# Optimization experiments

Hardware: AMD Instinct MI355X
Metric: run time of the kernel (lower is better)

Reference implementation:

```python
import jax, jax.numpy as jnp
import numpy as np

RADII = np.array([0.5, 1.0, 1.5, 2.0], dtype=np.float32)
SIGMA = 0.5          # gaussian radial-function width (= radius spacing)
EPS = 1e-8
N_SH = 9             # real spherical harmonics up to l=2
N_BASIS = len(RADII) * N_SH


def real_sh_l2(u):
    """Real spherical harmonics l=0,1,2 of unit vectors u[..., 3] -> [..., 9]."""
    x, y, z = u[..., 0], u[..., 1], u[..., 2]
    one = jnp.ones_like(x)
    return jnp.stack([
        0.28209479 * one,
        0.48860251 * x, 0.48860251 * y, 0.48860251 * z,
        1.09254843 * x * y,
        1.09254843 * y * z,
        0.31539157 * (3.0 * z * z - 1.0),
        1.09254843 * x * z,
        0.54627421 * (x * x - y * y),
    ], axis=-1)


def setup_inputs() -> dict:
    key = jax.random.key(0)
    k1, k2, k3, k4, k5 = jax.random.split(key, 5)
    n, c_in, d_out, b, a = 4, 32, 32, 8192, 32
    inp = jax.random.normal(k1, (n, c_in, b), jnp.float32)
    coords = jax.random.uniform(k2, (n, b, 3), jnp.float32) * 4.0
    neighbors = jax.random.randint(k3, (n, b, a), 0, b)
    relative_mask = jax.random.uniform(k4, (n, b, a), jnp.float32)
    W = jax.random.normal(k5, (d_out, c_in, N_BASIS), jnp.float32) / np.sqrt(c_in * N_BASIS)
    return {"input": inp, "coords": coords, "relative_mask": relative_mask,
            "W": W, "neighbors": neighbors}


def reference(input, coords, relative_mask, W, neighbors):
    n, c, b = input.shape
    idx_n = jnp.arange(n)[:, None, None]                     # [n,1,1]
    # neighbor difference matrix: coords[neighbors] - coords  -> [n,b,a,3]
    neigh_xyz = coords[idx_n, neighbors]
    diff = neigh_xyz - coords[:, :, None, :]
    r = jnp.linalg.norm(diff, axis=-1)                       # [n,b,a]
    u = diff / (r[..., None] + EPS)
    Y = real_sh_l2(u)                                        # [n,b,a,9]
    radii = jnp.asarray(RADII)
    rb = jnp.exp(-((r[..., None] - radii) / SIGMA) ** 2)     # [n,b,a,4]
    basis = (rb[..., :, None] * Y[..., None, :]).reshape(r.shape + (-1,))  # [n,b,a,36]
    # neighbor feature matrix: input[n, :, neighbors[n,b,a]] -> [n,b,a,c]
    feat = input[idx_n, :, neighbors]
    # relative_mask multiplies k over (n,b,a) == masking gathered features
    feat = feat * relative_mask[..., None]
    # fused form of: k[d,c,n,b,a] = sum_k basis[n,b,a,k] W[d,c,k];
    # out[n,d,b] = sum_{c,a} feat[n,b,a,c] * k[d,c,n,b,a]
    M = jnp.einsum('nbac,nbak->nbck', feat, basis)           # [n,b,c,36]
    return jnp.einsum('nbck,dck->ndb', M, W)
```

## Files before the change

kernel.cpp:

```cpp
#include <hip/hip_runtime.h>
#include <hip/hip_bf16.h>


typedef _Float16 f16x8 __attribute__((ext_vector_type(8)));
typedef _Float16 f16x4 __attribute__((ext_vector_type(4)));
typedef __fp16   h16x2 __attribute__((ext_vector_type(2)));
typedef float    f32x4 __attribute__((ext_vector_type(4)));
typedef unsigned int u32;

__device__ __forceinline__ u32 pk16(float a, float b) {
    union { h16x2 v; u32 u; } cv;
    cv.v = __builtin_amdgcn_cvt_pkrtz(a, b);
    return cv.u;
}

__global__ __launch_bounds__(256) void prep_kernel(
    const float* __restrict__ inp, const float* __restrict__ W,
    float* __restrict__ inp_t, unsigned short* __restrict__ Wfrag)
{
    if (blockIdx.x < 1024) {
        __shared__ float T[32][33];
        const int n  = blockIdx.x >> 8;
        const int b0 = (blockIdx.x & 255) << 5;
        const int bx = threadIdx.x & 31;
        const int cy = threadIdx.x >> 5;
        #pragma unroll
        for (int r = 0; r < 4; ++r) {
            const int cc = cy + r * 8;
            T[bx][cc] = inp[((n << 5) + cc) * 8192 + b0 + bx];
        }
        __syncthreads();
        #pragma unroll
        for (int r = 0; r < 4; ++r) {
            const int by = cy + r * 8;
            inp_t[((n << 13) + b0 + by) * 32 + bx] = T[by][bx];
        }
    } else {
        const int t = (blockIdx.x - 1024) * 256 + threadIdx.x;
        if (t < 36 * 2 * 64 * 8) {
            const int j  = t & 7;
            const int l  = (t >> 3) & 63;
            const int dt = (t >> 9) & 1;
            const int kt = t >> 10;
            const int d  = dt * 16 + (l & 15);
            const int c  = ((l >> 4) << 3) + j;
            const _Float16 hv = (_Float16)W[d * 1152 + c * 36 + kt];
            Wfrag[t] = __builtin_bit_cast(unsigned short, hv);
        }
    }
}

__global__ __launch_bounds__(256, 3) void se3_main(
    const float* __restrict__ inp_t, const float* __restrict__ coords,
    const float* __restrict__ rmask, const int* __restrict__ neigh,
    const unsigned short* __restrict__ Wfrag, float* __restrict__ out)
{
    __shared__ __align__(16) unsigned short Mb_s[36 * 580];
    __shared__ __align__(16) unsigned short bas[4][37 * 36];
    __shared__ int idxs[16][32];

    const int tid  = threadIdx.x;
    const int lane = tid & 63;
    const int w    = tid >> 6;
    const int l15  = lane & 15;
    const int q    = lane >> 4;
    const int a_   = lane & 31;
    const int h_   = lane >> 5;

    const int blk = blockIdx.x;
    const int n_  = (blk & 7) >> 1;
    const int pos = ((blk >> 3) << 1) | (blk & 1);
    const int b0  = pos << 4;
    const int gp0 = (n_ << 13) | b0;
    const int nbase_pt = n_ << 13;
    const float* __restrict__ inp_n = inp_t + ((size_t)n_ << 18);

    unsigned short* basw = &bas[w][0];

    const int ph0 = 2 * l15;
    const int ph1 = (l15 < 2) ? (32 + 2 * l15) : (2 * l15 - 3);
    const int ph2 = (l15 < 4) ? (29 + 2 * l15) : 36;
    const int offB0 = ph0 * 36 + (q << 3);
    const int offB1 = ph1 * 36 + (q << 3);
    const int offB2 = ph2 * 36 + (q << 3);

    #pragma unroll 1
    for (int pw = 0; pw < 4; ++pw) {
        const int p  = (w << 2) | pw;
        const int gp = gp0 + p;

        const int   abase = (gp << 5) | a_;
        const int   idx   = neigh[abase];
        const float msk   = rmask[abase];
        const float cx = coords[gp * 3 + 0];
        const float cy = coords[gp * 3 + 1];
        const float cz = coords[gp * 3 + 2];
        const int   nb = nbase_pt + idx;
        const float dx = coords[nb * 3 + 0] - cx;
        const float dy = coords[nb * 3 + 1] - cy;
        const float dz = coords[nb * 3 + 2] - cz;
        const float r   = sqrtf(dx * dx + dy * dy + dz * dz);
        const float inv = 1.0f / (r + 1e-8f);
        const float x = dx * inv, y = dy * inv, z = dz * inv;
        float Yv[9];
        Yv[0] = 0.28209479f;
        Yv[1] = 0.48860251f * x;
        Yv[2] = 0.48860251f * y;
        Yv[3] = 0.48860251f * z;
        Yv[4] = 1.09254843f * x * y;
        Yv[5] = 1.09254843f * y * z;
        Yv[6] = 0.31539157f * (3.0f * z * z - 1.0f);
        Yv[7] = 1.09254843f * x * z;
        Yv[8] = 0.54627421f * (x * x - y * y);
        const float t0 = (r - 0.5f) * 2.0f;
        const float t1 = (r - 1.0f) * 2.0f;
        const float t2 = (r - 1.5f) * 2.0f;
        const float t3 = (r - 2.0f) * 2.0f;
        const float rb0 = __expf(-t0 * t0) * msk;
        const float rb1 = __expf(-t1 * t1) * msk;
        const float rb2 = __expf(-t2 * t2) * msk;
        const float rb3 = __expf(-t3 * t3) * msk;

        if (lane < 32) idxs[p][a_] = idx;

        const float rbA = h_ ? rb2 : rb0;
        const float rbB = h_ ? rb3 : rb1;
        #pragma unroll
        for (int t = 0; t < 18; ++t) {
            const float v = (t < 9) ? rbA * Yv[t] : rbB * Yv[t - 9];
            const _Float16 hv = (_Float16)v;
            basw[(2 * t + h_) * 36 + a_] = __builtin_bit_cast(unsigned short, hv);
        }

        int ridx[8];
        #pragma unroll
        for (int j = 0; j < 8; ++j) ridx[j] = idxs[p][(q << 3) + j];
        float fv0[8], fv1[8];
        #pragma unroll
        for (int j = 0; j < 8; ++j) {
            const float* rp2 = inp_n + (((unsigned)ridx[j]) << 5) + l15;
            fv0[j] = rp2[0];
            fv1[j] = rp2[16];
        }
        union { f16x8 v; u32 u[4]; } af0, af1;
        #pragma unroll
        for (int j4 = 0; j4 < 4; ++j4) {
            af0.u[j4] = pk16(fv0[2 * j4], fv0[2 * j4 + 1]);
            af1.u[j4] = pk16(fv1[2 * j4], fv1[2 * j4 + 1]);
        }

        f16x4 blo, bhi;
        blo = *(const f16x4*)&basw[offB0]; bhi = *(const f16x4*)&basw[offB0 + 4];
        const f16x8 Bf0 = __builtin_shufflevector(blo, bhi, 0, 1, 2, 3, 4, 5, 6, 7);
        blo = *(const f16x4*)&basw[offB1]; bhi = *(const f16x4*)&basw[offB1 + 4];
        const f16x8 Bf1 = __builtin_shufflevector(blo, bhi, 0, 1, 2, 3, 4, 5, 6, 7);
        blo = *(const f16x4*)&basw[offB2]; bhi = *(const f16x4*)&basw[offB2 + 4];
        const f16x8 Bf2 = __builtin_shufflevector(blo, bhi, 0, 1, 2, 3, 4, 5, 6, 7);

        const f32x4 z4 = {0.0f, 0.0f, 0.0f, 0.0f};
        f32x4 D00 = __builtin_amdgcn_mfma_f32_16x16x32_f16(af0.v, Bf0, z4, 0, 0, 0);
        f32x4 D01 = __builtin_amdgcn_mfma_f32_16x16x32_f16(af0.v, Bf1, z4, 0, 0, 0);
        f32x4 D02 = __builtin_amdgcn_mfma_f32_16x16x32_f16(af0.v, Bf2, z4, 0, 0, 0);
        f32x4 D10 = __builtin_amdgcn_mfma_f32_16x16x32_f16(af1.v, Bf0, z4, 0, 0, 0);
        f32x4 D11 = __builtin_amdgcn_mfma_f32_16x16x32_f16(af1.v, Bf1, z4, 0, 0, 0);
        f32x4 D12 = __builtin_amdgcn_mfma_f32_16x16x32_f16(af1.v, Bf2, z4, 0, 0, 0);

        {
            const int rowp = p * 36 + (q << 2);
            const int b_0 = (0 * 16 + l15) * 580 + rowp;
            const int b_1 = (1 * 16 + l15) * 580 + rowp;
            *(u32*)&Mb_s[b_0]          = pk16(D00[0], D00[1]);
            *(u32*)&Mb_s[b_0 + 2]      = pk16(D00[2], D00[3]);
            *(u32*)&Mb_s[b_0 + 16]     = pk16(D10[0], D10[1]);
            *(u32*)&Mb_s[b_0 + 18]     = pk16(D10[2], D10[3]);
            *(u32*)&Mb_s[b_1]          = pk16(D01[0], D01[1]);
            *(u32*)&Mb_s[b_1 + 2]      = pk16(D01[2], D01[3]);
            *(u32*)&Mb_s[b_1 + 16]     = pk16(D11[0], D11[1]);
            *(u32*)&Mb_s[b_1 + 18]     = pk16(D11[2], D11[3]);
            if (l15 < 4) {
                const int b_2 = (32 + l15) * 580 + rowp;
                *(u32*)&Mb_s[b_2]      = pk16(D02[0], D02[1]);
                *(u32*)&Mb_s[b_2 + 2]  = pk16(D02[2], D02[3]);
                *(u32*)&Mb_s[b_2 + 16] = pk16(D12[0], D12[1]);
                *(u32*)&Mb_s[b_2 + 18] = pk16(D12[2], D12[3]);
            }
        }
    }
    __syncthreads();

    {
        const int dt  = w >> 1;
        const int kh2 = w & 1;
        f32x4 acc2 = {0.0f, 0.0f, 0.0f, 0.0f};
        const int kt0 = kh2 * 18;
        #pragma unroll 2
        for (int kt = kt0; kt < kt0 + 18; ++kt) {
            const f16x8 af = *(const f16x8*)&Wfrag[((size_t)((kt * 2 + dt) * 64 + lane)) << 3];
            const int mbase = kt * 580 + l15 * 36 + (q << 3);
            const f16x4 mlo = *(const f16x4*)&Mb_s[mbase];
            const f16x4 mhi = *(const f16x4*)&Mb_s[mbase + 4];
            const f16x8 bf  = __builtin_shufflevector(mlo, mhi, 0, 1, 2, 3, 4, 5, 6, 7);
            acc2 = __builtin_amdgcn_mfma_f32_16x16x32_f16(af, bf, acc2, 0, 0, 0);
        }
        __syncthreads();
        float* Cp = reinterpret_cast<float*>(Mb_s);
        *(f32x4*)&Cp[(w * 64 + lane) * 4] = acc2;
    }
    __syncthreads();

    if (w < 2) {
        const float* Cp = reinterpret_cast<const float*>(Mb_s);
        const int dt2 = w;
        const f32x4 s0 = *(const f32x4*)&Cp[((dt2 * 2 + 0) * 64 + lane) * 4];
        const f32x4 s1 = *(const f32x4*)&Cp[((dt2 * 2 + 1) * 64 + lane) * 4];
        const int drow = dt2 * 16 + (lane >> 4) * 4;
        const int col  = b0 + (lane & 15);
        #pragma unroll
        for (int rr = 0; rr < 4; ++rr) {
            out[(((n_ << 5) + drow + rr) << 13) + col] = s0[rr] + s1[rr];
        }
    }
}

extern "C" void kernel_launch(void* const* d_in, const int* in_sizes, int n_in,
                              void* d_out, int out_size, void* d_ws, size_t ws_size,
                              hipStream_t stream)
{
    const float* inp    = (const float*)d_in[0];
    const float* coords = (const float*)d_in[1];
    const float* rmask  = (const float*)d_in[2];
    const float* W      = (const float*)d_in[3];
    const int*   neigh  = (const int*)d_in[4];
    float*       outp   = (float*)d_out;

    float*          inp_t = (float*)d_ws;
    unsigned short* Wfrag = (unsigned short*)((char*)d_ws + (4u << 20));

    prep_kernel<<<1168, 256, 0, stream>>>(inp, W, inp_t, Wfrag);
    se3_main<<<2048, 256, 0, stream>>>(inp_t, coords, rmask, neigh, Wfrag, outp);
}
```

Before: 104.2 us.

## Use 512-thread blocks with two points per wave and 4-way K split

Blocks grow to 8 waves, each handling two points instead of looping over four. All feature and coordinate loads for both points are issued up front, so gather latency overlaps with the geometry math. The second GEMM stage splits K four ways instead of two, and a dedicated LDS buffer for partial sums removes one barrier. The cost is more registers per thread under the 512-thread launch bound, plus extra LDS.

```diff
diff --git a/kernel.cpp b/kernel.cpp
--- a/kernel.cpp
+++ b/kernel.cpp
@@ -12,6 +12,36 @@
     union { h16x2 v; u32 u; } cv;
     cv.v = __builtin_amdgcn_cvt_pkrtz(a, b);
     return cv.u;
+}
+__device__ __forceinline__ unsigned short f16bits(float v) {
+    const _Float16 hv = (_Float16)v;
+    return __builtin_bit_cast(unsigned short, hv);
+}
+
+__device__ __forceinline__ void geom(float dx, float dy, float dz, float msk, int h_,
+                                     float Y[9], float& rbA, float& rbB) {
+    const float r   = sqrtf(dx * dx + dy * dy + dz * dz);
+    const float inv = 1.0f / (r + 1e-8f);
+    const float x = dx * inv, y = dy * inv, z = dz * inv;
+    Y[0] = 0.28209479f;
+    Y[1] = 0.48860251f * x;
+    Y[2] = 0.48860251f * y;
+    Y[3] = 0.48860251f * z;
+    Y[4] = 1.09254843f * x * y;
+    Y[5] = 1.09254843f * y * z;
+    Y[6] = 0.31539157f * (3.0f * z * z - 1.0f);
+    Y[7] = 1.09254843f * x * z;
+    Y[8] = 0.54627421f * (x * x - y * y);
+    const float t0 = (r - 0.5f) * 2.0f;
+    const float t1 = (r - 1.0f) * 2.0f;
+    const float t2 = (r - 1.5f) * 2.0f;
+    const float t3 = (r - 2.0f) * 2.0f;
+    const float rb0 = __expf(-t0 * t0) * msk;
+    const float rb1 = __expf(-t1 * t1) * msk;
+    const float rb2 = __expf(-t2 * t2) * msk;
+    const float rb3 = __expf(-t3 * t3) * msk;
+    rbA = h_ ? rb2 : rb0;
+    rbB = h_ ? rb3 : rb1;
 }
 
 __global__ __launch_bounds__(256) void prep_kernel(
@@ -44,20 +74,20 @@
             const int kt = t >> 10;
             const int d  = dt * 16 + (l & 15);
             const int c  = ((l >> 4) << 3) + j;
-            const _Float16 hv = (_Float16)W[d * 1152 + c * 36 + kt];
-            Wfrag[t] = __builtin_bit_cast(unsigned short, hv);
-        }
-    }
-}
-
-__global__ __launch_bounds__(256, 3) void se3_main(
+            Wfrag[t] = f16bits(W[d * 1152 + c * 36 + kt]);
+        }
+    }
+}
+
+__global__ __launch_bounds__(512, 4) void se3_main(
     const float* __restrict__ inp_t, const float* __restrict__ coords,
     const float* __restrict__ rmask, const int* __restrict__ neigh,
     const unsigned short* __restrict__ Wfrag, float* __restrict__ out)
 {
     __shared__ __align__(16) unsigned short Mb_s[36 * 580];
-    __shared__ __align__(16) unsigned short bas[4][37 * 36];
+    __shared__ __align__(16) unsigned short bas[8][37 * 36];
     __shared__ int idxs[16][32];
+    __shared__ __align__(16) float Cp[8 * 64 * 4];
 
     const int tid  = threadIdx.x;
     const int lane = tid & 63;
@@ -84,117 +114,136 @@
     const int offB1 = ph1 * 36 + (q << 3);
     const int offB2 = ph2 * 36 + (q << 3);
 
-    #pragma unroll 1
-    for (int pw = 0; pw < 4; ++pw) {
-        const int p  = (w << 2) | pw;
-        const int gp = gp0 + p;
-
-        const int   abase = (gp << 5) | a_;
-        const int   idx   = neigh[abase];
-        const float msk   = rmask[abase];
-        const float cx = coords[gp * 3 + 0];
-        const float cy = coords[gp * 3 + 1];
-        const float cz = coords[gp * 3 + 2];
-        const int   nb = nbase_pt + idx;
-        const float dx = coords[nb * 3 + 0] - cx;
-        const float dy = coords[nb * 3 + 1] - cy;
-        const float dz = coords[nb * 3 + 2] - cz;
-        const float r   = sqrtf(dx * dx + dy * dy + dz * dz);
-        const float inv = 1.0f / (r + 1e-8f);
-        const float x = dx * inv, y = dy * inv, z = dz * inv;
-        float Yv[9];
-        Yv[0] = 0.28209479f;
-        Yv[1] = 0.48860251f * x;
-        Yv[2] = 0.48860251f * y;
-        Yv[3] = 0.48860251f * z;
-        Yv[4] = 1.09254843f * x * y;
-        Yv[5] = 1.09254843f * y * z;
-        Yv[6] = 0.31539157f * (3.0f * z * z - 1.0f);
-        Yv[7] = 1.09254843f * x * z;
-        Yv[8] = 0.54627421f * (x * x - y * y);
-        const float t0 = (r - 0.5f) * 2.0f;
-        const float t1 = (r - 1.0f) * 2.0f;
-        const float t2 = (r - 1.5f) * 2.0f;
-        const float t3 = (r - 2.0f) * 2.0f;
-        const float rb0 = __expf(-t0 * t0) * msk;
-        const float rb1 = __expf(-t1 * t1) * msk;
-        const float rb2 = __expf(-t2 * t2) * msk;
-        const float rb3 = __expf(-t3 * t3) * msk;
-
-        if (lane < 32) idxs[p][a_] = idx;
-
-        const float rbA = h_ ? rb2 : rb0;
-        const float rbB = h_ ? rb3 : rb1;
-        #pragma unroll
-        for (int t = 0; t < 18; ++t) {
-            const float v = (t < 9) ? rbA * Yv[t] : rbB * Yv[t - 9];
-            const _Float16 hv = (_Float16)v;
-            basw[(2 * t + h_) * 36 + a_] = __builtin_bit_cast(unsigned short, hv);
-        }
-
-        int ridx[8];
-        #pragma unroll
-        for (int j = 0; j < 8; ++j) ridx[j] = idxs[p][(q << 3) + j];
-        float fv0[8], fv1[8];
-        #pragma unroll
-        for (int j = 0; j < 8; ++j) {
-            const float* rp2 = inp_n + (((unsigned)ridx[j]) << 5) + l15;
-            fv0[j] = rp2[0];
-            fv1[j] = rp2[16];
-        }
-        union { f16x8 v; u32 u[4]; } af0, af1;
-        #pragma unroll
-        for (int j4 = 0; j4 < 4; ++j4) {
-            af0.u[j4] = pk16(fv0[2 * j4], fv0[2 * j4 + 1]);
-            af1.u[j4] = pk16(fv1[2 * j4], fv1[2 * j4 + 1]);
-        }
-
-        f16x4 blo, bhi;
-        blo = *(const f16x4*)&basw[offB0]; bhi = *(const f16x4*)&basw[offB0 + 4];
-        const f16x8 Bf0 = __builtin_shufflevector(blo, bhi, 0, 1, 2, 3, 4, 5, 6, 7);
-        blo = *(const f16x4*)&basw[offB1]; bhi = *(const f16x4*)&basw[offB1 + 4];
-        const f16x8 Bf1 = __builtin_shufflevector(blo, bhi, 0, 1, 2, 3, 4, 5, 6, 7);
-        blo = *(const f16x4*)&basw[offB2]; bhi = *(const f16x4*)&basw[offB2 + 4];
-        const f16x8 Bf2 = __builtin_shufflevector(blo, bhi, 0, 1, 2, 3, 4, 5, 6, 7);
-
-        const f32x4 z4 = {0.0f, 0.0f, 0.0f, 0.0f};
-        f32x4 D00 = __builtin_amdgcn_mfma_f32_16x16x32_f16(af0.v, Bf0, z4, 0, 0, 0);
-        f32x4 D01 = __builtin_amdgcn_mfma_f32_16x16x32_f16(af0.v, Bf1, z4, 0, 0, 0);
-        f32x4 D02 = __builtin_amdgcn_mfma_f32_16x16x32_f16(af0.v, Bf2, z4, 0, 0, 0);
-        f32x4 D10 = __builtin_amdgcn_mfma_f32_16x16x32_f16(af1.v, Bf0, z4, 0, 0, 0);
-        f32x4 D11 = __builtin_amdgcn_mfma_f32_16x16x32_f16(af1.v, Bf1, z4, 0, 0, 0);
-        f32x4 D12 = __builtin_amdgcn_mfma_f32_16x16x32_f16(af1.v, Bf2, z4, 0, 0, 0);
-
-        {
-            const int rowp = p * 36 + (q << 2);
-            const int b_0 = (0 * 16 + l15) * 580 + rowp;
-            const int b_1 = (1 * 16 + l15) * 580 + rowp;
-            *(u32*)&Mb_s[b_0]          = pk16(D00[0], D00[1]);
-            *(u32*)&Mb_s[b_0 + 2]      = pk16(D00[2], D00[3]);
-            *(u32*)&Mb_s[b_0 + 16]     = pk16(D10[0], D10[1]);
-            *(u32*)&Mb_s[b_0 + 18]     = pk16(D10[2], D10[3]);
-            *(u32*)&Mb_s[b_1]          = pk16(D01[0], D01[1]);
-            *(u32*)&Mb_s[b_1 + 2]      = pk16(D01[2], D01[3]);
-            *(u32*)&Mb_s[b_1 + 16]     = pk16(D11[0], D11[1]);
-            *(u32*)&Mb_s[b_1 + 18]     = pk16(D11[2], D11[3]);
-            if (l15 < 4) {
-                const int b_2 = (32 + l15) * 580 + rowp;
-                *(u32*)&Mb_s[b_2]      = pk16(D02[0], D02[1]);
-                *(u32*)&Mb_s[b_2 + 2]  = pk16(D02[2], D02[3]);
-                *(u32*)&Mb_s[b_2 + 16] = pk16(D12[0], D12[1]);
-                *(u32*)&Mb_s[b_2 + 18] = pk16(D12[2], D12[3]);
-            }
+    const int pA = w << 1, pB = pA | 1;
+    const int gpA = gp0 + pA, gpB = gp0 + pB;
+
+    const int   idxA = neigh[(gpA << 5) | a_];
+    const int   idxB = neigh[(gpB << 5) | a_];
+    const float mskA = rmask[(gpA << 5) | a_];
+    const float mskB = rmask[(gpB << 5) | a_];
+    const float cxA = coords[gpA * 3 + 0], cyA = coords[gpA * 3 + 1], czA = coords[gpA * 3 + 2];
+    const float cxB = coords[gpB * 3 + 0], cyB = coords[gpB * 3 + 1], czB = coords[gpB * 3 + 2];
+    if (lane < 32) { idxs[pA][a_] = idxA; idxs[pB][a_] = idxB; }
+    const int nbA = (nbase_pt + idxA) * 3;
+    const int nbB = (nbase_pt + idxB) * 3;
+    const float dxA = coords[nbA + 0] - cxA, dyA = coords[nbA + 1] - cyA, dzA = coords[nbA + 2] - czA;
+    const float dxB = coords[nbB + 0] - cxB, dyB = coords[nbB + 1] - cyB, dzB = coords[nbB + 2] - czB;
+
+    float fA0[8], fA1[8], fB0[8], fB1[8];
+    #pragma unroll
+    for (int j = 0; j < 8; ++j) {
+        const int ri = idxs[pA][(q << 3) + j];
+        const float* rp = inp_n + (((unsigned)ri) << 5) + l15;
+        fA0[j] = rp[0]; fA1[j] = rp[16];
+    }
+    #pragma unroll
+    for (int j = 0; j < 8; ++j) {
+        const int ri = idxs[pB][(q << 3) + j];
+        const float* rp = inp_n + (((unsigned)ri) << 5) + l15;
+        fB0[j] = rp[0]; fB1[j] = rp[16];
+    }
+
+    float YA[9], YB[9], rbA_A, rbB_A, rbA_B, rbB_B;
+    geom(dxA, dyA, dzA, mskA, h_, YA, rbA_A, rbB_A);
+    geom(dxB, dyB, dzB, mskB, h_, YB, rbA_B, rbB_B);
+
+    #pragma unroll
+    for (int t = 0; t < 18; ++t) {
+        const float v = (t < 9) ? rbA_A * YA[t] : rbB_A * YA[t - 9];
+        basw[(2 * t + h_) * 36 + a_] = f16bits(v);
+    }
+
+    f16x4 blo, bhi;
+    blo = *(const f16x4*)&basw[offB0]; bhi = *(const f16x4*)&basw[offB0 + 4];
+    const f16x8 BfA0 = __builtin_shufflevector(blo, bhi, 0, 1, 2, 3, 4, 5, 6, 7);
+    blo = *(const f16x4*)&basw[offB1]; bhi = *(const f16x4*)&basw[offB1 + 4];
+    const f16x8 BfA1 = __builtin_shufflevector(blo, bhi, 0, 1, 2, 3, 4, 5, 6, 7);
+    blo = *(const f16x4*)&basw[offB2]; bhi = *(const f16x4*)&basw[offB2 + 4];
+    const f16x8 BfA2 = __builtin_shufflevector(blo, bhi, 0, 1, 2, 3, 4, 5, 6, 7);
+
+    union { f16x8 v; u32 u[4]; } afA0, afA1, afB0, afB1;
+    #pragma unroll
+    for (int j4 = 0; j4 < 4; ++j4) {
+        afA0.u[j4] = pk16(fA0[2 * j4], fA0[2 * j4 + 1]);
+        afA1.u[j4] = pk16(fA1[2 * j4], fA1[2 * j4 + 1]);
+    }
+    const f32x4 z4 = {0.0f, 0.0f, 0.0f, 0.0f};
+    f32x4 DA00 = __builtin_amdgcn_mfma_f32_16x16x32_f16(afA0.v, BfA0, z4, 0, 0, 0);
+    f32x4 DA01 = __builtin_amdgcn_mfma_f32_16x16x32_f16(afA0.v, BfA1, z4, 0, 0, 0);
+    f32x4 DA02 = __builtin_amdgcn_mfma_f32_16x16x32_f16(afA0.v, BfA2, z4, 0, 0, 0);
+    f32x4 DA10 = __builtin_amdgcn_mfma_f32_16x16x32_f16(afA1.v, BfA0, z4, 0, 0, 0);
+    f32x4 DA11 = __builtin_amdgcn_mfma_f32_16x16x32_f16(afA1.v, BfA1, z4, 0, 0, 0);
+    f32x4 DA12 = __builtin_amdgcn_mfma_f32_16x16x32_f16(afA1.v, BfA2, z4, 0, 0, 0);
+
+    #pragma unroll
+    for (int t = 0; t < 18; ++t) {
+        const float v = (t < 9) ? rbA_B * YB[t] : rbB_B * YB[t - 9];
+        basw[(2 * t + h_) * 36 + a_] = f16bits(v);
+    }
+    blo = *(const f16x4*)&basw[offB0]; bhi = *(const f16x4*)&basw[offB0 + 4];
+    const f16x8 BfB0 = __builtin_shufflevector(blo, bhi, 0, 1, 2, 3, 4, 5, 6, 7);
+    blo = *(const f16x4*)&basw[offB1]; bhi = *(const f16x4*)&basw[offB1 + 4];
+    const f16x8 BfB1 = __builtin_shufflevector(blo, bhi, 0, 1, 2, 3, 4, 5, 6, 7);
+    blo = *(const f16x4*)&basw[offB2]; bhi = *(const f16x4*)&basw[offB2 + 4];
+    const f16x8 BfB2 = __builtin_shufflevector(blo, bhi, 0, 1, 2, 3, 4, 5, 6, 7);
+
+    #pragma unroll
+    for (int j4 = 0; j4 < 4; ++j4) {
+        afB0.u[j4] = pk16(fB0[2 * j4], fB0[2 * j4 + 1]);
+        afB1.u[j4] = pk16(fB1[2 * j4], fB1[2 * j4 + 1]);
+    }
+    f32x4 DB00 = __builtin_amdgcn_mfma_f32_16x16x32_f16(afB0.v, BfB0, z4, 0, 0, 0);
+    f32x4 DB01 = __builtin_amdgcn_mfma_f32_16x16x32_f16(afB0.v, BfB1, z4, 0, 0, 0);
+    f32x4 DB02 = __builtin_amdgcn_mfma_f32_16x16x32_f16(afB0.v, BfB2, z4, 0, 0, 0);
+    f32x4 DB10 = __builtin_amdgcn_mfma_f32_16x16x32_f16(afB1.v, BfB0, z4, 0, 0, 0);
+    f32x4 DB11 = __builtin_amdgcn_mfma_f32_16x16x32_f16(afB1.v, BfB1, z4, 0, 0, 0);
+    f32x4 DB12 = __builtin_amdgcn_mfma_f32_16x16x32_f16(afB1.v, BfB2, z4, 0, 0, 0);
+
+    {
+        const int rowpA = pA * 36 + (q << 2);
+        const int a0 = l15 * 580 + rowpA;
+        const int a1 = (16 + l15) * 580 + rowpA;
+        *(u32*)&Mb_s[a0]      = pk16(DA00[0], DA00[1]);
+        *(u32*)&Mb_s[a0 + 2]  = pk16(DA00[2], DA00[3]);
+        *(u32*)&Mb_s[a0 + 16] = pk16(DA10[0], DA10[1]);
+        *(u32*)&Mb_s[a0 + 18] = pk16(DA10[2], DA10[3]);
+        *(u32*)&Mb_s[a1]      = pk16(DA01[0], DA01[1]);
+        *(u32*)&Mb_s[a1 + 2]  = pk16(DA01[2], DA01[3]);
+        *(u32*)&Mb_s[a1 + 16] = pk16(DA11[0], DA11[1]);
+        *(u32*)&Mb_s[a1 + 18] = pk16(DA11[2], DA11[3]);
+        const int rowpB = pB * 36 + (q << 2);
+        const int c0 = l15 * 580 + rowpB;
+        const int c1 = (16 + l15) * 580 + rowpB;
+        *(u32*)&Mb_s[c0]      = pk16(DB00[0], DB00[1]);
+        *(u32*)&Mb_s[c0 + 2]  = pk16(DB00[2], DB00[3]);
+        *(u32*)&Mb_s[c0 + 16] = pk16(DB10[0], DB10[1]);
+        *(u32*)&Mb_s[c0 + 18] = pk16(DB10[2], DB10[3]);
+        *(u32*)&Mb_s[c1]      = pk16(DB01[0], DB01[1]);
+        *(u32*)&Mb_s[c1 + 2]  = pk16(DB01[2], DB01[3]);
+        *(u32*)&Mb_s[c1 + 16] = pk16(DB11[0], DB11[1]);
+        *(u32*)&Mb_s[c1 + 18] = pk16(DB11[2], DB11[3]);
+        if (l15 < 4) {
+            const int a2 = (32 + l15) * 580 + rowpA;
+            *(u32*)&Mb_s[a2]      = pk16(DA02[0], DA02[1]);
+            *(u32*)&Mb_s[a2 + 2]  = pk16(DA02[2], DA02[3]);
+            *(u32*)&Mb_s[a2 + 16] = pk16(DA12[0], DA12[1]);
+            *(u32*)&Mb_s[a2 + 18] = pk16(DA12[2], DA12[3]);
+            const int c2 = (32 + l15) * 580 + rowpB;
+            *(u32*)&Mb_s[c2]      = pk16(DB02[0], DB02[1]);
+            *(u32*)&Mb_s[c2 + 2]  = pk16(DB02[2], DB02[3]);
+            *(u32*)&Mb_s[c2 + 16] = pk16(DB12[0], DB12[1]);
+            *(u32*)&Mb_s[c2 + 18] = pk16(DB12[2], DB12[3]);
         }
     }
     __syncthreads();
 
     {
-        const int dt  = w >> 1;
-        const int kh2 = w & 1;
+        const int dt  = w >> 2;
+        const int seg = w & 3;
         f32x4 acc2 = {0.0f, 0.0f, 0.0f, 0.0f};
-        const int kt0 = kh2 * 18;
-        #pragma unroll 2
-        for (int kt = kt0; kt < kt0 + 18; ++kt) {
+        const int kt0 = seg * 9;
+        #pragma unroll 3
+        for (int kt = kt0; kt < kt0 + 9; ++kt) {
             const f16x8 af = *(const f16x8*)&Wfrag[((size_t)((kt * 2 + dt) * 64 + lane)) << 3];
             const int mbase = kt * 580 + l15 * 36 + (q << 3);
             const f16x4 mlo = *(const f16x4*)&Mb_s[mbase];
@@ -202,22 +251,23 @@
             const f16x8 bf  = __builtin_shufflevector(mlo, mhi, 0, 1, 2, 3, 4, 5, 6, 7);
             acc2 = __builtin_amdgcn_mfma_f32_16x16x32_f16(af, bf, acc2, 0, 0, 0);
         }
-        __syncthreads();
-        float* Cp = reinterpret_cast<float*>(Mb_s);
         *(f32x4*)&Cp[(w * 64 + lane) * 4] = acc2;
     }
     __syncthreads();
 
     if (w < 2) {
-        const float* Cp = reinterpret_cast<const float*>(Mb_s);
         const int dt2 = w;
-        const f32x4 s0 = *(const f32x4*)&Cp[((dt2 * 2 + 0) * 64 + lane) * 4];
-        const f32x4 s1 = *(const f32x4*)&Cp[((dt2 * 2 + 1) * 64 + lane) * 4];
+        f32x4 s = *(const f32x4*)&Cp[((dt2 * 4 + 0) * 64 + lane) * 4];
+        #pragma unroll
+        for (int rphase = 1; rphase < 4; ++rphase) {
+            const f32x4 t = *(const f32x4*)&Cp[((dt2 * 4 + rphase) * 64 + lane) * 4];
+            s[0] += t[0]; s[1] += t[1]; s[2] += t[2]; s[3] += t[3];
+        }
         const int drow = dt2 * 16 + (lane >> 4) * 4;
         const int col  = b0 + (lane & 15);
         #pragma unroll
         for (int rr = 0; rr < 4; ++rr) {
-            out[(((n_ << 5) + drow + rr) << 13) + col] = s0[rr] + s1[rr];
+            out[(((n_ << 5) + drow + rr) << 13) + col] = s[rr];
         }
     }
 }
@@ -237,5 +287,5 @@
     unsigned short* Wfrag = (unsigned short*)((char*)d_ws + (4u << 20));
 
     prep_kernel<<<1168, 256, 0, stream>>>(inp, W, inp_t, Wfrag);
-    se3_main<<<2048, 256, 0, stream>>>(inp_t, coords, rmask, neigh, Wfrag, outp);
-}
+    se3_main<<<2048, 512, 0, stream>>>(inp_t, coords, rmask, neigh, Wfrag, outp);
+}
```

Result: faster. 93.04 us (-10.7%).

## Assign one point per wave with 8-point blocks and 4-way split-K reduction

Applied to the files above, without the earlier changes.

Blocks now hold 8 points and 8 waves, so each wave handles a single point instead of looping over four. Grid size doubles and LDS per block roughly halves. The W-projection GEMM is split four ways along K across waves, with a 4-way partial-sum reduction through shared memory. Neighbor feature gathers are issued before the geometry math to overlap their latency. In exchange, half the MFMA N columns in the second GEMM carry duplicated data, and the W fragments are reloaded for fewer points per block.

```diff
diff --git a/kernel.cpp b/kernel.cpp
--- a/kernel.cpp
+++ b/kernel.cpp
@@ -12,6 +12,36 @@
     union { h16x2 v; u32 u; } cv;
     cv.v = __builtin_amdgcn_cvt_pkrtz(a, b);
     return cv.u;
+}
+__device__ __forceinline__ unsigned short f16bits(float v) {
+    const _Float16 hv = (_Float16)v;
+    return __builtin_bit_cast(unsigned short, hv);
+}
+
+__device__ __forceinline__ void geom(float dx, float dy, float dz, float msk, int h_,
+                                     float Y[9], float& rbA, float& rbB) {
+    const float r   = sqrtf(dx * dx + dy * dy + dz * dz);
+    const float inv = 1.0f / (r + 1e-8f);
+    const float x = dx * inv, y = dy * inv, z = dz * inv;
+    Y[0] = 0.28209479f;
+    Y[1] = 0.48860251f * x;
+    Y[2] = 0.48860251f * y;
+    Y[3] = 0.48860251f * z;
+    Y[4] = 1.09254843f * x * y;
+    Y[5] = 1.09254843f * y * z;
+    Y[6] = 0.31539157f * (3.0f * z * z - 1.0f);
+    Y[7] = 1.09254843f * x * z;
+    Y[8] = 0.54627421f * (x * x - y * y);
+    const float t0 = (r - 0.5f) * 2.0f;
+    const float t1 = (r - 1.0f) * 2.0f;
+    const float t2 = (r - 1.5f) * 2.0f;
+    const float t3 = (r - 2.0f) * 2.0f;
+    const float rb0 = __expf(-t0 * t0) * msk;
+    const float rb1 = __expf(-t1 * t1) * msk;
+    const float rb2 = __expf(-t2 * t2) * msk;
+    const float rb3 = __expf(-t3 * t3) * msk;
+    rbA = h_ ? rb2 : rb0;
+    rbB = h_ ? rb3 : rb1;
 }
 
 __global__ __launch_bounds__(256) void prep_kernel(
@@ -44,20 +74,19 @@
             const int kt = t >> 10;
             const int d  = dt * 16 + (l & 15);
             const int c  = ((l >> 4) << 3) + j;
-            const _Float16 hv = (_Float16)W[d * 1152 + c * 36 + kt];
-            Wfrag[t] = __builtin_bit_cast(unsigned short, hv);
-        }
-    }
-}
-
-__global__ __launch_bounds__(256, 3) void se3_main(
+            Wfrag[t] = f16bits(W[d * 1152 + c * 36 + kt]);
+        }
+    }
+}
+
+__global__ __launch_bounds__(512, 6) void se3_main(
     const float* __restrict__ inp_t, const float* __restrict__ coords,
     const float* __restrict__ rmask, const int* __restrict__ neigh,
     const unsigned short* __restrict__ Wfrag, float* __restrict__ out)
 {
-    __shared__ __align__(16) unsigned short Mb_s[36 * 580];
-    __shared__ __align__(16) unsigned short bas[4][37 * 36];
-    __shared__ int idxs[16][32];
+    __shared__ __align__(16) unsigned short Mb_s[36 * 292];
+    __shared__ __align__(16) unsigned short bas[8][37 * 36];
+    __shared__ int idxs[8][32];
 
     const int tid  = threadIdx.x;
     const int lane = tid & 63;
@@ -70,7 +99,7 @@
     const int blk = blockIdx.x;
     const int n_  = (blk & 7) >> 1;
     const int pos = ((blk >> 3) << 1) | (blk & 1);
-    const int b0  = pos << 4;
+    const int b0  = pos << 3;
     const int gp0 = (n_ << 13) | b0;
     const int nbase_pt = n_ << 13;
     const float* __restrict__ inp_n = inp_t + ((size_t)n_ << 18);
@@ -84,140 +113,110 @@
     const int offB1 = ph1 * 36 + (q << 3);
     const int offB2 = ph2 * 36 + (q << 3);
 
-    #pragma unroll 1
-    for (int pw = 0; pw < 4; ++pw) {
-        const int p  = (w << 2) | pw;
-        const int gp = gp0 + p;
-
-        const int   abase = (gp << 5) | a_;
-        const int   idx   = neigh[abase];
-        const float msk   = rmask[abase];
-        const float cx = coords[gp * 3 + 0];
-        const float cy = coords[gp * 3 + 1];
-        const float cz = coords[gp * 3 + 2];
-        const int   nb = nbase_pt + idx;
-        const float dx = coords[nb * 3 + 0] - cx;
-        const float dy = coords[nb * 3 + 1] - cy;
-        const float dz = coords[nb * 3 + 2] - cz;
-        const float r   = sqrtf(dx * dx + dy * dy + dz * dz);
-        const float inv = 1.0f / (r + 1e-8f);
-        const float x = dx * inv, y = dy * inv, z = dz * inv;
-        float Yv[9];
-        Yv[0] = 0.28209479f;
-        Yv[1] = 0.48860251f * x;
-        Yv[2] = 0.48860251f * y;
-        Yv[3] = 0.48860251f * z;
-        Yv[4] = 1.09254843f * x * y;
-        Yv[5] = 1.09254843f * y * z;
-        Yv[6] = 0.31539157f * (3.0f * z * z - 1.0f);
-        Yv[7] = 1.09254843f * x * z;
-        Yv[8] = 0.54627421f * (x * x - y * y);
-        const float t0 = (r - 0.5f) * 2.0f;
-        const float t1 = (r - 1.0f) * 2.0f;
-        const float t2 = (r - 1.5f) * 2.0f;
-        const float t3 = (r - 2.0f) * 2.0f;
-        const float rb0 = __expf(-t0 * t0) * msk;
-        const float rb1 = __expf(-t1 * t1) * msk;
-        const float rb2 = __expf(-t2 * t2) * msk;
-        const float rb3 = __expf(-t3 * t3) * msk;
-
-        if (lane < 32) idxs[p][a_] = idx;
-
-        const float rbA = h_ ? rb2 : rb0;
-        const float rbB = h_ ? rb3 : rb1;
-        #pragma unroll
-        for (int t = 0; t < 18; ++t) {
-            const float v = (t < 9) ? rbA * Yv[t] : rbB * Yv[t - 9];
-            const _Float16 hv = (_Float16)v;
-            basw[(2 * t + h_) * 36 + a_] = __builtin_bit_cast(unsigned short, hv);
-        }
-
-        int ridx[8];
-        #pragma unroll
-        for (int j = 0; j < 8; ++j) ridx[j] = idxs[p][(q << 3) + j];
-        float fv0[8], fv1[8];
-        #pragma unroll
-        for (int j = 0; j < 8; ++j) {
-            const float* rp2 = inp_n + (((unsigned)ridx[j]) << 5) + l15;
-            fv0[j] = rp2[0];
-            fv1[j] = rp2[16];
-        }
-        union { f16x8 v; u32 u[4]; } af0, af1;
-        #pragma unroll
-        for (int j4 = 0; j4 < 4; ++j4) {
-            af0.u[j4] = pk16(fv0[2 * j4], fv0[2 * j4 + 1]);
-            af1.u[j4] = pk16(fv1[2 * j4], fv1[2 * j4 + 1]);
-        }
-
-        f16x4 blo, bhi;
-        blo = *(const f16x4*)&basw[offB0]; bhi = *(const f16x4*)&basw[offB0 + 4];
-        const f16x8 Bf0 = __builtin_shufflevector(blo, bhi, 0, 1, 2, 3, 4, 5, 6, 7);
-        blo = *(const f16x4*)&basw[offB1]; bhi = *(const f16x4*)&basw[offB1 + 4];
-        const f16x8 Bf1 = __builtin_shufflevector(blo, bhi, 0, 1, 2, 3, 4, 5, 6, 7);
-        blo = *(const f16x4*)&basw[offB2]; bhi = *(const f16x4*)&basw[offB2 + 4];
-        const f16x8 Bf2 = __builtin_shufflevector(blo, bhi, 0, 1, 2, 3, 4, 5, 6, 7);
-
-        const f32x4 z4 = {0.0f, 0.0f, 0.0f, 0.0f};
-        f32x4 D00 = __builtin_amdgcn_mfma_f32_16x16x32_f16(af0.v, Bf0, z4, 0, 0, 0);
-        f32x4 D01 = __builtin_amdgcn_mfma_f32_16x16x32_f16(af0.v, Bf1, z4, 0, 0, 0);
-        f32x4 D02 = __builtin_amdgcn_mfma_f32_16x16x32_f16(af0.v, Bf2, z4, 0, 0, 0);
-        f32x4 D10 = __builtin_amdgcn_mfma_f32_16x16x32_f16(af1.v, Bf0, z4, 0, 0, 0);
-        f32x4 D11 = __builtin_amdgcn_mfma_f32_16x16x32_f16(af1.v, Bf1, z4, 0, 0, 0);
-        f32x4 D12 = __builtin_amdgcn_mfma_f32_16x16x32_f16(af1.v, Bf2, z4, 0, 0, 0);
-
-        {
-            const int rowp = p * 36 + (q << 2);
-            const int b_0 = (0 * 16 + l15) * 580 + rowp;
-            const int b_1 = (1 * 16 + l15) * 580 + rowp;
-            *(u32*)&Mb_s[b_0]          = pk16(D00[0], D00[1]);
-            *(u32*)&Mb_s[b_0 + 2]      = pk16(D00[2], D00[3]);
-            *(u32*)&Mb_s[b_0 + 16]     = pk16(D10[0], D10[1]);
-            *(u32*)&Mb_s[b_0 + 18]     = pk16(D10[2], D10[3]);
-            *(u32*)&Mb_s[b_1]          = pk16(D01[0], D01[1]);
-            *(u32*)&Mb_s[b_1 + 2]      = pk16(D01[2], D01[3]);
-            *(u32*)&Mb_s[b_1 + 16]     = pk16(D11[0], D11[1]);
-            *(u32*)&Mb_s[b_1 + 18]     = pk16(D11[2], D11[3]);
-            if (l15 < 4) {
-                const int b_2 = (32 + l15) * 580 + rowp;
-                *(u32*)&Mb_s[b_2]      = pk16(D02[0], D02[1]);
-                *(u32*)&Mb_s[b_2 + 2]  = pk16(D02[2], D02[3]);
-                *(u32*)&Mb_s[b_2 + 16] = pk16(D12[0], D12[1]);
-                *(u32*)&Mb_s[b_2 + 18] = pk16(D12[2], D12[3]);
-            }
+    const int p  = w;
+    const int gp = gp0 + p;
+
+    const int   idx = neigh[(gp << 5) | a_];
+    const float msk = rmask[(gp << 5) | a_];
+    const float cx = coords[gp * 3 + 0], cy = coords[gp * 3 + 1], cz = coords[gp * 3 + 2];
+    if (lane < 32) idxs[p][a_] = idx;
+    const int nb = (nbase_pt + idx) * 3;
+    const float dx = coords[nb + 0] - cx, dy = coords[nb + 1] - cy, dz = coords[nb + 2] - cz;
+
+    float f0[8], f1[8];
+    #pragma unroll
+    for (int j = 0; j < 8; ++j) {
+        const int ri = idxs[p][(q << 3) + j];
+        const float* rp = inp_n + (((unsigned)ri) << 5) + l15;
+        f0[j] = rp[0];
+        f1[j] = rp[16];
+    }
+
+    float Y[9], rbA, rbB;
+    geom(dx, dy, dz, msk, h_, Y, rbA, rbB);
+
+    #pragma unroll
+    for (int t = 0; t < 18; ++t) {
+        const float v = (t < 9) ? rbA * Y[t] : rbB * Y[t - 9];
+        basw[(2 * t + h_) * 36 + a_] = f16bits(v);
+    }
+
+    f16x4 blo, bhi;
+    blo = *(const f16x4*)&basw[offB0]; bhi = *(const f16x4*)&basw[offB0 + 4];
+    const f16x8 Bf0 = __builtin_shufflevector(blo, bhi, 0, 1, 2, 3, 4, 5, 6, 7);
+    blo = *(const f16x4*)&basw[offB1]; bhi = *(const f16x4*)&basw[offB1 + 4];
+    const f16x8 Bf1 = __builtin_shufflevector(blo, bhi, 0, 1, 2, 3, 4, 5, 6, 7);
+    blo = *(const f16x4*)&basw[offB2]; bhi = *(const f16x4*)&basw[offB2 + 4];
+    const f16x8 Bf2 = __builtin_shufflevector(blo, bhi, 0, 1, 2, 3, 4, 5, 6, 7);
+
+    union { f16x8 v; u32 u[4]; } af0, af1;
+    #pragma unroll
+    for (int j4 = 0; j4 < 4; ++j4) {
+        af0.u[j4] = pk16(f0[2 * j4], f0[2 * j4 + 1]);
+        af1.u[j4] = pk16(f1[2 * j4], f1[2 * j4 + 1]);
+    }
+    const f32x4 z4 = {0.0f, 0.0f, 0.0f, 0.0f};
+    f32x4 D00 = __builtin_amdgcn_mfma_f32_16x16x32_f16(af0.v, Bf0, z4, 0, 0, 0);
+    f32x4 D01 = __builtin_amdgcn_mfma_f32_16x16x32_f16(af0.v, Bf1, z4, 0, 0, 0);
+    f32x4 D02 = __builtin_amdgcn_mfma_f32_16x16x32_f16(af0.v, Bf2, z4, 0, 0, 0);
+    f32x4 D10 = __builtin_amdgcn_mfma_f32_16x16x32_f16(af1.v, Bf0, z4, 0, 0, 0);
+    f32x4 D11 = __builtin_amdgcn_mfma_f32_16x16x32_f16(af1.v, Bf1, z4, 0, 0, 0);
+    f32x4 D12 = __builtin_amdgcn_mfma_f32_16x16x32_f16(af1.v, Bf2, z4, 0, 0, 0);
+
+    {
+        const int rowp = p * 36 + (q << 2);
+        const int b_0 = l15 * 292 + rowp;
+        const int b_1 = (16 + l15) * 292 + rowp;
+        *(u32*)&Mb_s[b_0]      = pk16(D00[0], D00[1]);
+        *(u32*)&Mb_s[b_0 + 2]  = pk16(D00[2], D00[3]);
+        *(u32*)&Mb_s[b_0 + 16] = pk16(D10[0], D10[1]);
+        *(u32*)&Mb_s[b_0 + 18] = pk16(D10[2], D10[3]);
+        *(u32*)&Mb_s[b_1]      = pk16(D01[0], D01[1]);
+        *(u32*)&Mb_s[b_1 + 2]  = pk16(D01[2], D01[3]);
+        *(u32*)&Mb_s[b_1 + 16] = pk16(D11[0], D11[1]);
+        *(u32*)&Mb_s[b_1 + 18] = pk16(D11[2], D11[3]);
+        if (l15 < 4) {
+            const int b_2 = (32 + l15) * 292 + rowp;
+            *(u32*)&Mb_s[b_2]      = pk16(D02[0], D02[1]);
+            *(u32*)&Mb_s[b_2 + 2]  = pk16(D02[2], D02[3]);
+            *(u32*)&Mb_s[b_2 + 16] = pk16(D12[0], D12[1]);
+            *(u32*)&Mb_s[b_2 + 18] = pk16(D12[2], D12[3]);
         }
     }
     __syncthreads();
 
+    float* Cp = reinterpret_cast<float*>(bas);
     {
-        const int dt  = w >> 1;
-        const int kh2 = w & 1;
+        const int dt  = w >> 2;
+        const int seg = w & 3;
         f32x4 acc2 = {0.0f, 0.0f, 0.0f, 0.0f};
-        const int kt0 = kh2 * 18;
-        #pragma unroll 2
-        for (int kt = kt0; kt < kt0 + 18; ++kt) {
+        const int kt0 = seg * 9;
+        #pragma unroll 3
+        for (int kt = kt0; kt < kt0 + 9; ++kt) {
             const f16x8 af = *(const f16x8*)&Wfrag[((size_t)((kt * 2 + dt) * 64 + lane)) << 3];
-            const int mbase = kt * 580 + l15 * 36 + (q << 3);
+            const int mbase = kt * 292 + (l15 & 7) * 36 + (q << 3);
             const f16x4 mlo = *(const f16x4*)&Mb_s[mbase];
             const f16x4 mhi = *(const f16x4*)&Mb_s[mbase + 4];
             const f16x8 bf  = __builtin_shufflevector(mlo, mhi, 0, 1, 2, 3, 4, 5, 6, 7);
             acc2 = __builtin_amdgcn_mfma_f32_16x16x32_f16(af, bf, acc2, 0, 0, 0);
         }
-        __syncthreads();
-        float* Cp = reinterpret_cast<float*>(Mb_s);
         *(f32x4*)&Cp[(w * 64 + lane) * 4] = acc2;
     }
     __syncthreads();
 
-    if (w < 2) {
-        const float* Cp = reinterpret_cast<const float*>(Mb_s);
+    if (w < 2 && l15 < 8) {
         const int dt2 = w;
-        const f32x4 s0 = *(const f32x4*)&Cp[((dt2 * 2 + 0) * 64 + lane) * 4];
-        const f32x4 s1 = *(const f32x4*)&Cp[((dt2 * 2 + 1) * 64 + lane) * 4];
+        f32x4 s = *(const f32x4*)&Cp[((dt2 * 4 + 0) * 64 + lane) * 4];
+        #pragma unroll
+        for (int rphase = 1; rphase < 4; ++rphase) {
+            const f32x4 t = *(const f32x4*)&Cp[((dt2 * 4 + rphase) * 64 + lane) * 4];
+            s[0] += t[0]; s[1] += t[1]; s[2] += t[2]; s[3] += t[3];
+        }
         const int drow = dt2 * 16 + (lane >> 4) * 4;
-        const int col  = b0 + (lane & 15);
+        const int col  = b0 + l15;
         #pragma unroll
         for (int rr = 0; rr < 4; ++rr) {
-            out[(((n_ << 5) + drow + rr) << 13) + col] = s0[rr] + s1[rr];
+            out[(((n_ << 5) + drow + rr) << 13) + col] = s[rr];
         }
     }
 }
@@ -237,5 +236,5 @@
     unsigned short* Wfrag = (unsigned short*)((char*)d_ws + (4u << 20));
 
     prep_kernel<<<1168, 256, 0, stream>>>(inp, W, inp_t, Wfrag);
-    se3_main<<<2048, 256, 0, stream>>>(inp_t, coords, rmask, neigh, Wfrag, outp);
-}
+    se3_main<<<4096, 512, 0, stream>>>(inp_t, coords, rmask, neigh, Wfrag, outp);
+}
```

Result: faster. 97.00 us (-6.9%).
